# Kernel optimization log

Measured on AMD Instinct MI355X. Metric: run time of the kernel, lower is better.

The kernel has to match this reference:

```python
import jax, jax.numpy as jnp
import numpy as np

HIDDEN = 384
NDIM = 3
N_POINTS = 100000
N_SUPER = 2048
MAX_DEG = 32
RADIUS = 0.045
INPUT_DIM = 3


def _sincos_embed(coords):
    # ContinuousSincosEmbed: dim=384, ndim=3 -> 128 channels per spatial dim (64 sin + 64 cos)
    eff = HIDDEN // NDIM  # 128
    omega = jnp.arange(0, eff, 2, dtype=jnp.float32) / eff
    freq = 1.0 / (10000.0 ** omega)  # [eff//2]
    out = coords[..., None] * freq  # [..., ndim, eff//2]
    emb = jnp.concatenate([jnp.sin(out), jnp.cos(out)], axis=-1)  # [..., ndim, eff]
    return emb.reshape(coords.shape[:-1] + (HIDDEN,))


def _radius_neighbors(pos, sn_idx):
    # numpy preprocessing equivalent of torch_geometric.nn.pool.radius with
    # max_num_neighbors=MAX_DEG; fixed-size padded [S, K] output + validity mask.
    nbr = np.zeros((N_SUPER, MAX_DEG), np.int32)
    mask = np.zeros((N_SUPER, MAX_DEG), bool)
    pos2 = (pos ** 2).sum(-1)
    r2 = RADIUS * RADIUS
    chunk = 128
    for i0 in range(0, N_SUPER, chunk):
        sp = pos[sn_idx[i0:i0 + chunk]]
        d2 = (sp ** 2).sum(-1)[:, None] + pos2[None, :] - 2.0 * (sp @ pos.T)
        within = d2 <= r2
        for j in range(sp.shape[0]):
            idx = np.nonzero(within[j])[0][:MAX_DEG]
            nbr[i0 + j, :len(idx)] = idx
            mask[i0 + j, :len(idx)] = True
    return nbr, mask


def setup_inputs() -> dict:
    rng = np.random.default_rng(0)
    pos = rng.random((N_POINTS, NDIM)).astype(np.float32)
    sn_idx = np.sort(rng.choice(N_POINTS, N_SUPER, replace=False)).astype(np.int32)
    nbr, mask = _radius_neighbors(pos, sn_idx)
    key = jax.random.key(0)
    ks = jax.random.split(key, 6)
    s = 0.02  # truncnormal002 init scale
    return {
        "input_pos": jnp.asarray(pos),
        "input_feat": jax.random.normal(ks[0], (N_POINTS, INPUT_DIM), jnp.float32),
        "supernode_idx": jnp.asarray(sn_idx),
        "neighbor_idx": jnp.asarray(nbr),
        "neighbor_mask": jnp.asarray(mask),
        "W_in": jax.random.normal(ks[1], (INPUT_DIM, HIDDEN), jnp.float32) * s,
        "b_in": jnp.zeros((HIDDEN,), jnp.float32),
        "W1": jax.random.normal(ks[2], (2 * HIDDEN, HIDDEN), jnp.float32) * s,
        "b1": jnp.zeros((HIDDEN,), jnp.float32),
        "W2": jax.random.normal(ks[3], (HIDDEN, HIDDEN), jnp.float32) * s,
        "b2": jnp.zeros((HIDDEN,), jnp.float32),
        "W_proj": jax.random.normal(ks[4], (2 * HIDDEN, HIDDEN), jnp.float32) * s,
        "b_proj": jnp.zeros((HIDDEN,), jnp.float32),
    }


def reference(input_pos, input_feat, supernode_idx, neighbor_idx, neighbor_mask,
              W_in, b_in, W1, b1, W2, b2, W_proj, b_proj):
    # point embeddings: continuous sincos pos embed + input feature projection
    x = _sincos_embed(input_pos) + input_feat @ W_in + b_in          # [N, D]
    sn = x[supernode_idx]                                            # [S, D] supernode pos embed
    src = x[neighbor_idx]                                            # [S, K, D] gathered neighbors
    dst = jnp.broadcast_to(sn[:, None, :], src.shape)                # [S, K, D]
    h = jnp.concatenate([src, dst], axis=-1)                         # [S, K, 2D]
    # message MLP (Linear -> GELU(exact) -> Linear), as nn.GELU default
    h = jax.nn.gelu(h @ W1 + b1, approximate=False) @ W2 + b2        # [S, K, D]
    # masked mean == segment_csr(..., reduce='mean') over variable-degree edges
    m = neighbor_mask[..., None].astype(h.dtype)
    agg = (h * m).sum(axis=1) / jnp.maximum(m.sum(axis=1), 1.0)      # [S, D]
    # readd_supernode_pos: concat supernode pos embed, project 2D -> D
    out = jnp.concatenate([agg, sn], axis=-1) @ W_proj + b_proj      # [S, D]
    return out[None]                                                 # [1, S, D] (batch_size=1)
```

## Files before the change

### kernel.cpp

```cpp
#include <hip/hip_runtime.h>
#include <hip/hip_bf16.h>
#include <cstdint>

#define HIDDEN 384
#define NSUPER 2048
#define MAXDEG 32
#define FRAGS (12*24*64)
#define WBLK  (FRAGS*8)

typedef __attribute__((ext_vector_type(8))) short bf16x8;
typedef __attribute__((ext_vector_type(4))) float f32x4;

__device__ inline unsigned short f2bf(float f) {
    unsigned int u = __float_as_uint(f);
    return (unsigned short)((u + 0x7fffu + ((u >> 16) & 1u)) >> 16);
}
__device__ inline float b2f(unsigned short s) {
    return __uint_as_float(((unsigned int)s) << 16);
}
__device__ inline bf16x8 pack8(const float* v) {
    union { bf16x8 v8; unsigned short u[8]; } u;
    #pragma unroll
    for (int i = 0; i < 8; ++i) u.u[i] = f2bf(v[i]);
    return u.v8;
}
__device__ inline float gelu(float y) {
    const float y2 = y * y;
    const float m  = __expf(y * fmaf(-0.0713548163f, y2, -1.5957691216f));
    return y * (1.0f / (1.0f + m));
}

__global__ __launch_bounds__(256)
void prep(const float* __restrict__ W1, const float* __restrict__ W2,
          const float* __restrict__ Wp, const unsigned int* __restrict__ mask,
          const float* __restrict__ pos, const float* __restrict__ feat,
          const int* __restrict__ sn_idx,
          const float* __restrict__ W_in, const float* __restrict__ b_in,
          unsigned short* __restrict__ w1sf, unsigned short* __restrict__ w1df,
          unsigned short* __restrict__ w2f,  unsigned short* __restrict__ wpf,
          unsigned short* __restrict__ snxb, int* __restrict__ flag) {
    const int b = blockIdx.x;
    const int t = threadIdx.x;
    if (b == 360) {
        __shared__ int s;
        if (t == 0) s = 0;
        __syncthreads();
        int bad = 0;
        for (int i = t; i < 16384; i += 256)
            if (mask[i] > 1u) bad = 1;
        if (bad) s = 1;
        __syncthreads();
        if (t == 0) *flag = s;
        return;
    }
    if (b > 360) {
        __shared__ float W4[HIDDEN][4];
        __shared__ float P6[64][7];
        const int eb = b - 361;
        if (t < 64) {
            const int pi = sn_idx[eb*64 + t];
            P6[t][0]=pos[pi*3];  P6[t][1]=pos[pi*3+1];  P6[t][2]=pos[pi*3+2];
            P6[t][3]=feat[pi*3]; P6[t][4]=feat[pi*3+1]; P6[t][5]=feat[pi*3+2];
        }
        for (int d = t; d < HIDDEN; d += 256) {
            W4[d][0]=W_in[d]; W4[d][1]=W_in[HIDDEN+d];
            W4[d][2]=W_in[2*HIDDEN+d]; W4[d][3]=b_in[d];
        }
        __syncthreads();
        const int er = t >> 2, seg = t & 3;
        float frA[8], frB[8];
        #pragma unroll
        for (int i = 0; i < 8; ++i) {
            frA[i] = exp2f(-(float)(seg*8 + i)      * 0.2076205059304601f);
            frB[i] = exp2f(-(float)(32 + seg*8 + i) * 0.2076205059304601f);
        }
        const float f0 = P6[er][3], f1 = P6[er][4], f2 = P6[er][5];
        #pragma unroll
        for (int cc = 0; cc < 3; ++cc) {
            const float pc = P6[er][cc];
            float sL[8], sH[8], cL[8], cH[8];
            #pragma unroll
            for (int i = 0; i < 8; ++i) {
                const float aL = pc*frA[i], aH = pc*frB[i];
                sL[i]=__sinf(aL); sH[i]=__sinf(aH); cL[i]=__cosf(aL); cH[i]=__cosf(aH);
            }
            #pragma unroll
            for (int q = 0; q < 4; ++q) {
                const float* bb = (q==0)?sL:(q==1)?sH:(q==2)?cL:cH;
                const int blk = cc*4 + q;
                float v[8];
                #pragma unroll
                for (int i = 0; i < 8; ++i) {
                    const int dim = blk*32 + seg*8 + i;
                    const float4 wv = *(const float4*)W4[dim];
                    v[i] = fmaf(f0, wv.x, fmaf(f1, wv.y, fmaf(f2, wv.z, bb[i] + wv.w)));
                }
                *(bf16x8*)&snxb[(size_t)(eb*64 + er)*HIDDEN + blk*32 + seg*8] = pack8(v);
            }
        }
        return;
    }
    const int grp = b / 72, sub = b % 72;
    const float* W; unsigned short* out;
    switch (grp) {
        case 0: W = W1;              out = w1sf; break;
        case 1: W = W1 + 384*HIDDEN; out = w1df; break;
        case 2: W = W2;              out = w2f;  break;
        case 3: W = Wp;              out = wpf;  break;
        default:W = Wp + 384*HIDDEN; out = wpf + WBLK; break;
    }
    const int idx = sub * 256 + t;
    const int l   = idx & 63;
    const int frag= idx >> 6;
    const int nt  = frag % 24;
    const int kt  = frag / 24;
    const int col = nt * 16 + (l & 15);
    const int k0  = kt * 32 + (l >> 4) * 8;
    unsigned int pk[4];
    #pragma unroll
    for (int j = 0; j < 4; ++j) {
        unsigned int lo = f2bf(W[(k0 + 2*j)     * HIDDEN + col]);
        unsigned int hi = f2bf(W[(k0 + 2*j + 1) * HIDDEN + col]);
        pk[j] = lo | (hi << 16);
    }
    *reinterpret_cast<uint4*>(&out[(size_t)idx * 8]) =
        *reinterpret_cast<const uint4*>(pk);
}

__global__ __launch_bounds__(256, 2)
void k_mlp(const float* __restrict__ pos, const float* __restrict__ feat,
           const int* __restrict__ nbr_idx, const void* __restrict__ mask_raw,
           const int* __restrict__ mask_fmt,
           const float* __restrict__ W_in, const float* __restrict__ b_in,
           const unsigned short* __restrict__ snxb,
           const unsigned short* __restrict__ W1sf,
           const unsigned short* __restrict__ W1df,
           const float* __restrict__ b1,
           unsigned short* __restrict__ aggpre, float* __restrict__ cntf)
{
    __shared__ unsigned short G[4*12*64*8];
    __shared__ ushort4 WINTB[HIDDEN];
    __shared__ float PF[64][7];
    __shared__ float CNT[2];

    const int t  = threadIdx.x;
    const int bm = blockIdx.x;
    const int l = t & 63, ng = t >> 6, lg = l >> 4, l15 = l & 15;

    bf16x8 bA[6], bB[6];
    #define LOADB(dst, Wf, kt)                                                  \
        { const unsigned short* bp_ = &Wf[((size_t)((kt)*24 + ng*6)*64 + l)*8]; \
          _Pragma("unroll")                                                     \
          for (int nt_ = 0; nt_ < 6; ++nt_)                                     \
              dst[nt_] = *(const bf16x8*)(bp_ + (size_t)nt_*512); }
    #define AREAD(a_, kt)                                                       \
        { _Pragma("unroll")                                                     \
          for (int mt_ = 0; mt_ < 4; ++mt_)                                     \
              a_[mt_] = *(const bf16x8*)&G[(size_t)(((mt_*12 + (kt))*64) + l)*8]; }
    #define MFMA6(bfr, a_)                                                      \
        { __builtin_amdgcn_s_setprio(1);                                        \
          _Pragma("unroll")                                                     \
          for (int mt_ = 0; mt_ < 4; ++mt_)                                     \
              _Pragma("unroll")                                                 \
              for (int nt_ = 0; nt_ < 6; ++nt_)                                 \
                  acc[mt_][nt_] = __builtin_amdgcn_mfma_f32_16x16x32_bf16(      \
                      a_[mt_], bfr[nt_], acc[mt_][nt_], 0, 0, 0);               \
          __builtin_amdgcn_s_setprio(0); }

    if (t < 64) {
        const int e  = bm*64 + t;
        const int pi = nbr_idx[e];
        PF[t][0]=pos[pi*3];  PF[t][1]=pos[pi*3+1];  PF[t][2]=pos[pi*3+2];
        PF[t][3]=feat[pi*3]; PF[t][4]=feat[pi*3+1]; PF[t][5]=feat[pi*3+2];
        const int fmt = *mask_fmt;
        const int mv  = fmt ? (int)((const unsigned char*)mask_raw)[e]
                            : ((const int*)mask_raw)[e];
        PF[t][6] = mv ? 1.0f : 0.0f;
    }
    for (int d = t; d < HIDDEN; d += 256) {
        ushort4 wv;
        wv.x = f2bf(W_in[d]); wv.y = f2bf(W_in[HIDDEN+d]);
        wv.z = f2bf(W_in[2*HIDDEN+d]); wv.w = f2bf(b_in[d]);
        WINTB[d] = wv;
    }
    float b1r[6];
    #pragma unroll
    for (int nt = 0; nt < 6; ++nt) b1r[nt] = b1[ng*96 + nt*16 + l15];
    __syncthreads();
    if (t < 2) {
        float c = 0.f;
        for (int s = 0; s < 32; ++s) c += PF[t*32+s][6];
        CNT[t] = c;
    }

    const int er = t >> 2, seg = t & 3;
    float frA[8], frB[8];
    #pragma unroll
    for (int i = 0; i < 8; ++i) {
        frA[i] = exp2f(-(float)(seg*8 + i)      * 0.2076205059304601f);
        frB[i] = exp2f(-(float)(32 + seg*8 + i) * 0.2076205059304601f);
    }
    const float f0 = PF[er][3], f1 = PF[er][4], f2 = PF[er][5];
    const float pc0 = PF[er][0], pc1 = PF[er][1], pc2 = PF[er][2];
    const int slotbase = (er>>4)*12*64 + seg*16 + (er&15);

    #define EMB(kt_)                                                            \
        { const float pc = ((kt_)>>2)==0 ? pc0 : (((kt_)>>2)==1 ? pc1 : pc2);   \
          float v[8];                                                           \
          _Pragma("unroll")                                                     \
          for (int i = 0; i < 8; ++i) {                                         \
              const float fr = ((kt_)&1) ? frB[i] : frA[i];                     \
              const float aa = pc * fr;                                         \
              const float base = (((kt_)>>1)&1) ? __cosf(aa) : __sinf(aa);      \
              const ushort4 wv = WINTB[(kt_)*32 + seg*8 + i];                   \
              v[i] = fmaf(f0, b2f(wv.x), fmaf(f1, b2f(wv.y),                    \
                     fmaf(f2, b2f(wv.z), base + b2f(wv.w))));                   \
          }                                                                     \
          *(bf16x8*)&G[(size_t)(slotbase + (kt_)*64)*8] = pack8(v); }

    f32x4 acc[4][6];
    #pragma unroll
    for (int mt=0; mt<4; ++mt)
        #pragma unroll
        for (int nt=0; nt<6; ++nt) acc[mt][nt] = (f32x4){0.f,0.f,0.f,0.f};

    const unsigned short* snx0 = &snxb[(size_t)(bm*2 + 0)*HIDDEN];
    const unsigned short* snx1 = &snxb[(size_t)(bm*2 + 1)*HIDDEN];
    #pragma unroll
    for (int kt = 0; kt < 12; ++kt) {
        LOADB(bA, W1df, kt);
        bf16x8 s0 = *(const bf16x8*)&snx0[kt*32 + lg*8];
        bf16x8 s1 = *(const bf16x8*)&snx1[kt*32 + lg*8];
        EMB(kt);
        __builtin_amdgcn_s_setprio(1);
        #pragma unroll
        for (int nt = 0; nt < 6; ++nt) {
            acc[0][nt] = __builtin_amdgcn_mfma_f32_16x16x32_bf16(s0, bA[nt], acc[0][nt], 0,0,0);
            acc[1][nt] = __builtin_amdgcn_mfma_f32_16x16x32_bf16(s0, bA[nt], acc[1][nt], 0,0,0);
            acc[2][nt] = __builtin_amdgcn_mfma_f32_16x16x32_bf16(s1, bA[nt], acc[2][nt], 0,0,0);
            acc[3][nt] = __builtin_amdgcn_mfma_f32_16x16x32_bf16(s1, bA[nt], acc[3][nt], 0,0,0);
        }
        __builtin_amdgcn_s_setprio(0);
    }
    __syncthreads();

    LOADB(bA, W1sf, 0); LOADB(bB, W1sf, 1);
    #pragma unroll
    for (int kt = 0; kt < 12; kt += 2) {
        bf16x8 a[4];
        AREAD(a, kt);
        MFMA6(bA, a);
        if (kt + 2 < 12) LOADB(bA, W1sf, kt + 2);
        AREAD(a, kt + 1);
        MFMA6(bB, a);
        if (kt + 3 < 12) LOADB(bB, W1sf, kt + 3);
    }

    #pragma unroll
    for (int nt=0; nt<6; ++nt) {
        const int col = ng*96 + nt*16 + l15;
        const float bb1 = b1r[nt];
        float s0 = 0.f, s1 = 0.f;
        #pragma unroll
        for (int mt=0; mt<4; ++mt) {
            float p = 0.f;
            #pragma unroll
            for (int r=0; r<4; ++r)
                p += PF[mt*16 + lg*4 + r][6] * gelu(acc[mt][nt][r] + bb1);
            if (mt < 2) s0 += p; else s1 += p;
        }
        s0 += __shfl_xor(s0,16); s0 += __shfl_xor(s0,32);
        s1 += __shfl_xor(s1,16); s1 += __shfl_xor(s1,32);
        if (lg == 0) {
            const int sn0 = bm*2;
            aggpre[(size_t)sn0*HIDDEN + col]     = f2bf(s0 / fmaxf(CNT[0],1.f));
            aggpre[(size_t)(sn0+1)*HIDDEN + col] = f2bf(s1 / fmaxf(CNT[1],1.f));
        }
    }
    if (t < 2) cntf[bm*2 + t] = CNT[t];
    #undef LOADB
    #undef AREAD
    #undef MFMA6
    #undef EMB
}

__global__ __launch_bounds__(256)
void k_agg(const unsigned short* __restrict__ aggpre,
           const unsigned short* __restrict__ w2f,
           const float* __restrict__ b2, const float* __restrict__ cntf,
           unsigned short* __restrict__ aggb) {
    const int rg = blockIdx.x >> 2, cq = blockIdx.x & 3;
    const int t = threadIdx.x, w = t>>6, l = t&63, lg = l>>4, l15 = l&15;
    const int wgm = w>>1, wgn = w&1;
    const int r0 = rg*64 + wgm*32;
    const int ntb = cq*6 + wgn*3;
    f32x4 acc[2][3];
    #pragma unroll
    for (int mt=0; mt<2; ++mt)
        #pragma unroll
        for (int nt=0; nt<3; ++nt) acc[mt][nt] = (f32x4){0.f,0.f,0.f,0.f};
    #pragma unroll 2
    for (int kt = 0; kt < 12; ++kt) {
        bf16x8 a[2], bfr[3];
        const unsigned short* bpp = &w2f[((size_t)(kt*24 + ntb)*64 + l)*8];
        #pragma unroll
        for (int nt=0; nt<3; ++nt) bfr[nt] = *(const bf16x8*)(bpp + (size_t)nt*512);
        #pragma unroll
        for (int mt=0; mt<2; ++mt)
            a[mt] = *(const bf16x8*)&aggpre[(size_t)(r0 + mt*16 + l15)*HIDDEN + kt*32 + lg*8];
        #pragma unroll
        for (int mt=0; mt<2; ++mt)
            #pragma unroll
            for (int nt=0; nt<3; ++nt)
                acc[mt][nt] = __builtin_amdgcn_mfma_f32_16x16x32_bf16(a[mt], bfr[nt], acc[mt][nt], 0,0,0);
    }
    #pragma unroll
    for (int mt=0; mt<2; ++mt)
        #pragma unroll
        for (int nt=0; nt<3; ++nt) {
            const int col = cq*96 + wgn*48 + nt*16 + l15;
            const float bb = b2[col];
            #pragma unroll
            for (int r=0; r<4; ++r) {
                const int row = r0 + mt*16 + lg*4 + r;
                const float nz = (cntf[row] > 0.f) ? 1.f : 0.f;
                aggb[(size_t)row*HIDDEN + col] = f2bf(acc[mt][nt][r] + bb*nz);
            }
        }
}

__global__ __launch_bounds__(256)
void k_proj(const unsigned short* __restrict__ aggb,
            const unsigned short* __restrict__ snxb,
            const unsigned short* __restrict__ wpf,
            const float* __restrict__ bp, float* __restrict__ out) {
    const int rg = blockIdx.x >> 2, cq = blockIdx.x & 3;
    const int t = threadIdx.x, w = t>>6, l = t&63, lg = l>>4, l15 = l&15;
    const int wgm = w>>1, wgn = w&1;
    const int r0 = rg*64 + wgm*32;
    const int ntb = cq*6 + wgn*3;
    f32x4 acc[2][3];
    #pragma unroll
    for (int mt=0; mt<2; ++mt)
        #pragma unroll
        for (int nt=0; nt<3; ++nt) acc[mt][nt] = (f32x4){0.f,0.f,0.f,0.f};
    #pragma unroll 2
    for (int kt = 0; kt < 24; ++kt) {
        const unsigned short* Ab = (kt < 12) ? aggb : snxb;
        const unsigned short* Wb = (kt < 12) ? wpf  : wpf + WBLK;
        const int ktt = (kt < 12) ? kt : kt - 12;
        bf16x8 a[2], bfr[3];
        const unsigned short* bpp = &Wb[((size_t)(ktt*24 + ntb)*64 + l)*8];
        #pragma unroll
        for (int nt=0; nt<3; ++nt) bfr[nt] = *(const bf16x8*)(bpp + (size_t)nt*512);
        #pragma unroll
        for (int mt=0; mt<2; ++mt)
            a[mt] = *(const bf16x8*)&Ab[(size_t)(r0 + mt*16 + l15)*HIDDEN + ktt*32 + lg*8];
        #pragma unroll
        for (int mt=0; mt<2; ++mt)
            #pragma unroll
            for (int nt=0; nt<3; ++nt)
                acc[mt][nt] = __builtin_amdgcn_mfma_f32_16x16x32_bf16(a[mt], bfr[nt], acc[mt][nt], 0,0,0);
    }
    #pragma unroll
    for (int mt=0; mt<2; ++mt)
        #pragma unroll
        for (int nt=0; nt<3; ++nt) {
            const int col = cq*96 + wgn*48 + nt*16 + l15;
            #pragma unroll
            for (int r=0; r<4; ++r) {
                const int row = r0 + mt*16 + lg*4 + r;
                out[(size_t)row*HIDDEN + col] = acc[mt][nt][r] + bp[col];
            }
        }
}

extern "C" void kernel_launch(void* const* d_in, const int* in_sizes, int n_in,
                              void* d_out, int out_size, void* d_ws, size_t ws_size,
                              hipStream_t stream) {
    const float* pos   = (const float*)d_in[0];
    const float* feat  = (const float*)d_in[1];
    const int*   sn    = (const int*)d_in[2];
    const int*   nbr   = (const int*)d_in[3];
    const void*  mask  = d_in[4];
    const float* W_in  = (const float*)d_in[5];
    const float* b_in  = (const float*)d_in[6];
    const float* W1    = (const float*)d_in[7];
    const float* b1    = (const float*)d_in[8];
    const float* W2    = (const float*)d_in[9];
    const float* b2    = (const float*)d_in[10];
    const float* Wp    = (const float*)d_in[11];
    const float* bpv   = (const float*)d_in[12];
    float* out = (float*)d_out;

    char* base = (char*)d_ws;
    int* flag = (int*)base;
    unsigned short* w1sf = (unsigned short*)(base + 256);
    unsigned short* w1df = w1sf + WBLK;
    unsigned short* w2f  = w1df + WBLK;
    unsigned short* wpf  = w2f  + WBLK;
    unsigned short* snxb = wpf  + 2*(size_t)WBLK;
    unsigned short* aggb = snxb + (size_t)NSUPER*HIDDEN;
    unsigned short* aggp = aggb + (size_t)NSUPER*HIDDEN;
    float* cntf = (float*)(aggp + (size_t)NSUPER*HIDDEN);

    hipLaunchKernelGGL(prep, dim3(393), dim3(256), 0, stream,
                       W1, W2, Wp, (const unsigned int*)mask,
                       pos, feat, sn, W_in, b_in,
                       w1sf, w1df, w2f, wpf, snxb, flag);
    hipLaunchKernelGGL(k_mlp, dim3(1024), dim3(256), 0, stream,
                       pos, feat, nbr, mask, flag, W_in, b_in,
                       snxb, w1sf, w1df, b1, aggp, cntf);
    hipLaunchKernelGGL(k_agg, dim3(128), dim3(256), 0, stream,
                       aggp, w2f, b2, cntf, aggb);
    hipLaunchKernelGGL(k_proj, dim3(128), dim3(256), 0, stream,
                       aggb, snxb, wpf, bpv, out);
}
```

Measured before the change: 81.17 us.

## Precompute per-supernode dst projection once and widen MLP blocks to four supernodes

The dst half of the first layer (sn @ W1_dst + b1) is constant across a supernode's neighbors, so it moves into a separate small GEMM kernel run once per supernode and is added as a per-column bias after the src GEMM. This drops the redundant dst MFMAs that were repeated for every neighbor row. The MLP kernel now uses 512-thread blocks covering 4 supernodes (128 edges), with the embedding computed up front before a sync instead of interleaved with the dst MFMAs. The cost is an extra kernel launch, an fp32 dst buffer round trip, and a larger LDS footprint per block.

Result: slower. 87.21 us (+7.4%).

```diff
diff --git a/kernel.cpp b/kernel.cpp
--- a/kernel.cpp
+++ b/kernel.cpp
@@ -4,7 +4,6 @@
 
 #define HIDDEN 384
 #define NSUPER 2048
-#define MAXDEG 32
 #define FRAGS (12*24*64)
 #define WBLK  (FRAGS*8)
 
@@ -14,9 +13,6 @@
 __device__ inline unsigned short f2bf(float f) {
     unsigned int u = __float_as_uint(f);
     return (unsigned short)((u + 0x7fffu + ((u >> 16) & 1u)) >> 16);
-}
-__device__ inline float b2f(unsigned short s) {
-    return __uint_as_float(((unsigned int)s) << 16);
 }
 __device__ inline bf16x8 pack8(const float* v) {
     union { bf16x8 v8; unsigned short u[8]; } u;
@@ -119,44 +115,154 @@
     unsigned int pk[4];
     #pragma unroll
     for (int j = 0; j < 4; ++j) {
-        unsigned int lo = f2bf(W[(k0 + 2*j)     * HIDDEN + col]);
-        unsigned int hi = f2bf(W[(k0 + 2*j + 1) * HIDDEN + col]);
+        unsigned int lo = f2bf(W[(size_t)(k0 + 2*j)     * HIDDEN + col]);
+        unsigned int hi = f2bf(W[(size_t)(k0 + 2*j + 1) * HIDDEN + col]);
         pk[j] = lo | (hi << 16);
     }
     *reinterpret_cast<uint4*>(&out[(size_t)idx * 8]) =
         *reinterpret_cast<const uint4*>(pk);
 }
 
-__global__ __launch_bounds__(256, 2)
+__global__ __launch_bounds__(256)
+void k_dstv(const unsigned short* __restrict__ snxb,
+            const unsigned short* __restrict__ w1df,
+            const float* __restrict__ b1, float* __restrict__ dstv) {
+    const int rg = blockIdx.x >> 2, cq = blockIdx.x & 3;
+    const int t = threadIdx.x, w = t>>6, l = t&63, lg = l>>4, l15 = l&15;
+    const int wgm = w>>1, wgn = w&1;
+    const int r0 = rg*64 + wgm*32;
+    const int ntb = cq*6 + wgn*3;
+    f32x4 acc[2][3];
+    #pragma unroll
+    for (int mt=0; mt<2; ++mt)
+        #pragma unroll
+        for (int nt=0; nt<3; ++nt) acc[mt][nt] = (f32x4){0.f,0.f,0.f,0.f};
+    #pragma unroll 2
+    for (int kt = 0; kt < 12; ++kt) {
+        bf16x8 a[2], bfr[3];
+        const unsigned short* bpp = &w1df[((size_t)(kt*24 + ntb)*64 + l)*8];
+        #pragma unroll
+        for (int nt=0; nt<3; ++nt) bfr[nt] = *(const bf16x8*)(bpp + (size_t)nt*512);
+        #pragma unroll
+        for (int mt=0; mt<2; ++mt)
+            a[mt] = *(const bf16x8*)&snxb[(size_t)(r0 + mt*16 + l15)*HIDDEN + kt*32 + lg*8];
+        #pragma unroll
+        for (int mt=0; mt<2; ++mt)
+            #pragma unroll
+            for (int nt=0; nt<3; ++nt)
+                acc[mt][nt] = __builtin_amdgcn_mfma_f32_16x16x32_bf16(a[mt], bfr[nt], acc[mt][nt], 0,0,0);
+    }
+    #pragma unroll
+    for (int mt=0; mt<2; ++mt)
+        #pragma unroll
+        for (int nt=0; nt<3; ++nt) {
+            const int col = cq*96 + wgn*48 + nt*16 + l15;
+            #pragma unroll
+            for (int r=0; r<4; ++r) {
+                const int row = r0 + mt*16 + lg*4 + r;
+                dstv[(size_t)row*HIDDEN + col] = acc[mt][nt][r] + b1[col];
+            }
+        }
+}
+
+__global__ __launch_bounds__(512, 2)
 void k_mlp(const float* __restrict__ pos, const float* __restrict__ feat,
            const int* __restrict__ nbr_idx, const void* __restrict__ mask_raw,
            const int* __restrict__ mask_fmt,
            const float* __restrict__ W_in, const float* __restrict__ b_in,
-           const unsigned short* __restrict__ snxb,
+           const float* __restrict__ dstv,
            const unsigned short* __restrict__ W1sf,
-           const unsigned short* __restrict__ W1df,
-           const float* __restrict__ b1,
            unsigned short* __restrict__ aggpre, float* __restrict__ cntf)
 {
-    __shared__ unsigned short G[4*12*64*8];
+    __shared__ unsigned short G[8*12*64*8];
     __shared__ ushort4 WINTB[HIDDEN];
-    __shared__ float PF[64][7];
-    __shared__ float CNT[2];
+    __shared__ float PF[128][7];
+    __shared__ float CNT[4];
 
     const int t  = threadIdx.x;
     const int bm = blockIdx.x;
-    const int l = t & 63, ng = t >> 6, lg = l >> 4, l15 = l & 15;
+    const int l = t & 63, w = t >> 6;
+    const int mg = w >> 2, ng = w & 3;
+    const int lg = l >> 4, l15 = l & 15;
+
+    float dvreg[2][6];
+    #pragma unroll
+    for (int sl = 0; sl < 2; ++sl)
+        #pragma unroll
+        for (int nt = 0; nt < 6; ++nt)
+            dvreg[sl][nt] = dstv[(size_t)(bm*4 + mg*2 + sl)*HIDDEN + ng*96 + nt*16 + l15];
+
+    if (t < 128) {
+        const int e  = bm*128 + t;
+        const int pi = nbr_idx[e];
+        PF[t][0]=pos[pi*3];  PF[t][1]=pos[pi*3+1];  PF[t][2]=pos[pi*3+2];
+        PF[t][3]=feat[pi*3]; PF[t][4]=feat[pi*3+1]; PF[t][5]=feat[pi*3+2];
+        const int fmt = *mask_fmt;
+        const int mv  = fmt ? (int)((const unsigned char*)mask_raw)[e]
+                            : ((const int*)mask_raw)[e];
+        PF[t][6] = mv ? 1.0f : 0.0f;
+    }
+    if (t >= 128 && t < 128 + HIDDEN) {
+        const int d = t - 128;
+        ushort4 wv;
+        wv.x = f2bf(W_in[d]); wv.y = f2bf(W_in[HIDDEN+d]);
+        wv.z = f2bf(W_in[2*HIDDEN+d]); wv.w = f2bf(b_in[d]);
+        WINTB[d] = wv;
+    }
+    __syncthreads();
+    if (t < 4) {
+        float c = 0.f;
+        for (int s = 0; s < 32; ++s) c += PF[t*32+s][6];
+        CNT[t] = c;
+    }
+
+    {
+        const int er = t >> 2, seg = t & 3;
+        float frA[8], frB[8];
+        #pragma unroll
+        for (int i = 0; i < 8; ++i) {
+            frA[i] = exp2f(-(float)(seg*8 + i)      * 0.2076205059304601f);
+            frB[i] = exp2f(-(float)(32 + seg*8 + i) * 0.2076205059304601f);
+        }
+        const float f0 = PF[er][3], f1 = PF[er][4], f2 = PF[er][5];
+        const float pc0 = PF[er][0], pc1 = PF[er][1], pc2 = PF[er][2];
+        const int slotbase = (er>>4)*12*64 + seg*16 + (er&15);
+        #pragma unroll
+        for (int kt = 0; kt < 12; ++kt) {
+            const float pc = (kt>>2)==0 ? pc0 : ((kt>>2)==1 ? pc1 : pc2);
+            float v[8];
+            #pragma unroll
+            for (int i = 0; i < 8; ++i) {
+                const float fr = (kt&1) ? frB[i] : frA[i];
+                const float aa = pc * fr;
+                const float base = ((kt>>1)&1) ? __cosf(aa) : __sinf(aa);
+                const ushort4 wv = WINTB[kt*32 + seg*8 + i];
+                v[i] = fmaf(__uint_as_float((unsigned)wv.x<<16), f0,
+                       fmaf(__uint_as_float((unsigned)wv.y<<16), f1,
+                       fmaf(__uint_as_float((unsigned)wv.z<<16), f2,
+                            base + __uint_as_float((unsigned)wv.w<<16))));
+            }
+            *(bf16x8*)&G[(size_t)(slotbase + kt*64)*8] = pack8(v);
+        }
+    }
+    __syncthreads();
+
+    f32x4 acc[4][6];
+    #pragma unroll
+    for (int mt=0; mt<4; ++mt)
+        #pragma unroll
+        for (int nt=0; nt<6; ++nt) acc[mt][nt] = (f32x4){0.f,0.f,0.f,0.f};
 
     bf16x8 bA[6], bB[6];
-    #define LOADB(dst, Wf, kt)                                                  \
-        { const unsigned short* bp_ = &Wf[((size_t)((kt)*24 + ng*6)*64 + l)*8]; \
+    #define LOADB(dst, kt)                                                      \
+        { const unsigned short* bp_ = &W1sf[((size_t)((kt)*24 + ng*6)*64 + l)*8];\
           _Pragma("unroll")                                                     \
           for (int nt_ = 0; nt_ < 6; ++nt_)                                     \
               dst[nt_] = *(const bf16x8*)(bp_ + (size_t)nt_*512); }
     #define AREAD(a_, kt)                                                       \
         { _Pragma("unroll")                                                     \
           for (int mt_ = 0; mt_ < 4; ++mt_)                                     \
-              a_[mt_] = *(const bf16x8*)&G[(size_t)(((mt_*12 + (kt))*64) + l)*8]; }
+              a_[mt_] = *(const bf16x8*)&G[(size_t)((((mg*4 + mt_)*12 + (kt))*64) + l)*8]; }
     #define MFMA6(bfr, a_)                                                      \
         { __builtin_amdgcn_s_setprio(1);                                        \
           _Pragma("unroll")                                                     \
@@ -167,121 +273,49 @@
                       a_[mt_], bfr[nt_], acc[mt_][nt_], 0, 0, 0);               \
           __builtin_amdgcn_s_setprio(0); }
 
-    if (t < 64) {
-        const int e  = bm*64 + t;
-        const int pi = nbr_idx[e];
-        PF[t][0]=pos[pi*3];  PF[t][1]=pos[pi*3+1];  PF[t][2]=pos[pi*3+2];
-        PF[t][3]=feat[pi*3]; PF[t][4]=feat[pi*3+1]; PF[t][5]=feat[pi*3+2];
-        const int fmt = *mask_fmt;
-        const int mv  = fmt ? (int)((const unsigned char*)mask_raw)[e]
-                            : ((const int*)mask_raw)[e];
-        PF[t][6] = mv ? 1.0f : 0.0f;
-    }
-    for (int d = t; d < HIDDEN; d += 256) {
-        ushort4 wv;
-        wv.x = f2bf(W_in[d]); wv.y = f2bf(W_in[HIDDEN+d]);
-        wv.z = f2bf(W_in[2*HIDDEN+d]); wv.w = f2bf(b_in[d]);
-        WINTB[d] = wv;
-    }
-    float b1r[6];
-    #pragma unroll
-    for (int nt = 0; nt < 6; ++nt) b1r[nt] = b1[ng*96 + nt*16 + l15];
-    __syncthreads();
-    if (t < 2) {
-        float c = 0.f;
-        for (int s = 0; s < 32; ++s) c += PF[t*32+s][6];
-        CNT[t] = c;
-    }
-
-    const int er = t >> 2, seg = t & 3;
-    float frA[8], frB[8];
-    #pragma unroll
-    for (int i = 0; i < 8; ++i) {
-        frA[i] = exp2f(-(float)(seg*8 + i)      * 0.2076205059304601f);
-        frB[i] = exp2f(-(float)(32 + seg*8 + i) * 0.2076205059304601f);
-    }
-    const float f0 = PF[er][3], f1 = PF[er][4], f2 = PF[er][5];
-    const float pc0 = PF[er][0], pc1 = PF[er][1], pc2 = PF[er][2];
-    const int slotbase = (er>>4)*12*64 + seg*16 + (er&15);
-
-    #define EMB(kt_)                                                            \
-        { const float pc = ((kt_)>>2)==0 ? pc0 : (((kt_)>>2)==1 ? pc1 : pc2);   \
-          float v[8];                                                           \
-          _Pragma("unroll")                                                     \
-          for (int i = 0; i < 8; ++i) {                                         \
-              const float fr = ((kt_)&1) ? frB[i] : frA[i];                     \
-              const float aa = pc * fr;                                         \
-              const float base = (((kt_)>>1)&1) ? __cosf(aa) : __sinf(aa);      \
-              const ushort4 wv = WINTB[(kt_)*32 + seg*8 + i];                   \
-              v[i] = fmaf(f0, b2f(wv.x), fmaf(f1, b2f(wv.y),                    \
-                     fmaf(f2, b2f(wv.z), base + b2f(wv.w))));                   \
-          }                                                                     \
-          *(bf16x8*)&G[(size_t)(slotbase + (kt_)*64)*8] = pack8(v); }
-
-    f32x4 acc[4][6];
-    #pragma unroll
-    for (int mt=0; mt<4; ++mt)
-        #pragma unroll
-        for (int nt=0; nt<6; ++nt) acc[mt][nt] = (f32x4){0.f,0.f,0.f,0.f};
-
-    const unsigned short* snx0 = &snxb[(size_t)(bm*2 + 0)*HIDDEN];
-    const unsigned short* snx1 = &snxb[(size_t)(bm*2 + 1)*HIDDEN];
-    #pragma unroll
-    for (int kt = 0; kt < 12; ++kt) {
-        LOADB(bA, W1df, kt);
-        bf16x8 s0 = *(const bf16x8*)&snx0[kt*32 + lg*8];
-        bf16x8 s1 = *(const bf16x8*)&snx1[kt*32 + lg*8];
-        EMB(kt);
-        __builtin_amdgcn_s_setprio(1);
-        #pragma unroll
-        for (int nt = 0; nt < 6; ++nt) {
-            acc[0][nt] = __builtin_amdgcn_mfma_f32_16x16x32_bf16(s0, bA[nt], acc[0][nt], 0,0,0);
-            acc[1][nt] = __builtin_amdgcn_mfma_f32_16x16x32_bf16(s0, bA[nt], acc[1][nt], 0,0,0);
-            acc[2][nt] = __builtin_amdgcn_mfma_f32_16x16x32_bf16(s1, bA[nt], acc[2][nt], 0,0,0);
-            acc[3][nt] = __builtin_amdgcn_mfma_f32_16x16x32_bf16(s1, bA[nt], acc[3][nt], 0,0,0);
-        }
-        __builtin_amdgcn_s_setprio(0);
-    }
-    __syncthreads();
-
-    LOADB(bA, W1sf, 0); LOADB(bB, W1sf, 1);
+    LOADB(bA, 0); LOADB(bB, 1);
     #pragma unroll
     for (int kt = 0; kt < 12; kt += 2) {
         bf16x8 a[4];
         AREAD(a, kt);
         MFMA6(bA, a);
-        if (kt + 2 < 12) LOADB(bA, W1sf, kt + 2);
+        if (kt + 2 < 12) LOADB(bA, kt + 2);
         AREAD(a, kt + 1);
         MFMA6(bB, a);
-        if (kt + 3 < 12) LOADB(bB, W1sf, kt + 3);
-    }
-
+        if (kt + 3 < 12) LOADB(bB, kt + 3);
+    }
+
+    float mvr[4][4];
+    #pragma unroll
+    for (int mt=0; mt<4; ++mt)
+        #pragma unroll
+        for (int r=0; r<4; ++r)
+            mvr[mt][r] = PF[(mg*4 + mt)*16 + lg*4 + r][6];
     #pragma unroll
     for (int nt=0; nt<6; ++nt) {
         const int col = ng*96 + nt*16 + l15;
-        const float bb1 = b1r[nt];
         float s0 = 0.f, s1 = 0.f;
         #pragma unroll
         for (int mt=0; mt<4; ++mt) {
+            const float dv = dvreg[mt>>1][nt];
             float p = 0.f;
             #pragma unroll
             for (int r=0; r<4; ++r)
-                p += PF[mt*16 + lg*4 + r][6] * gelu(acc[mt][nt][r] + bb1);
+                p += mvr[mt][r] * gelu(acc[mt][nt][r] + dv);
             if (mt < 2) s0 += p; else s1 += p;
         }
         s0 += __shfl_xor(s0,16); s0 += __shfl_xor(s0,32);
         s1 += __shfl_xor(s1,16); s1 += __shfl_xor(s1,32);
         if (lg == 0) {
-            const int sn0 = bm*2;
-            aggpre[(size_t)sn0*HIDDEN + col]     = f2bf(s0 / fmaxf(CNT[0],1.f));
-            aggpre[(size_t)(sn0+1)*HIDDEN + col] = f2bf(s1 / fmaxf(CNT[1],1.f));
-        }
-    }
-    if (t < 2) cntf[bm*2 + t] = CNT[t];
+            const int sn0 = bm*4 + mg*2;
+            aggpre[(size_t)sn0*HIDDEN + col]     = f2bf(s0 / fmaxf(CNT[mg*2],1.f));
+            aggpre[(size_t)(sn0+1)*HIDDEN + col] = f2bf(s1 / fmaxf(CNT[mg*2+1],1.f));
+        }
+    }
+    if (t < 4) cntf[bm*4 + t] = CNT[t];
     #undef LOADB
     #undef AREAD
     #undef MFMA6
-    #undef EMB
 }
 
 __global__ __launch_bounds__(256)
@@ -403,14 +437,17 @@
     unsigned short* aggb = snxb + (size_t)NSUPER*HIDDEN;
     unsigned short* aggp = aggb + (size_t)NSUPER*HIDDEN;
     float* cntf = (float*)(aggp + (size_t)NSUPER*HIDDEN);
+    float* dstv = cntf + NSUPER;
 
     hipLaunchKernelGGL(prep, dim3(393), dim3(256), 0, stream,
                        W1, W2, Wp, (const unsigned int*)mask,
                        pos, feat, sn, W_in, b_in,
                        w1sf, w1df, w2f, wpf, snxb, flag);
-    hipLaunchKernelGGL(k_mlp, dim3(1024), dim3(256), 0, stream,
-                       pos, feat, nbr, mask, flag, W_in, b_in,
-                       snxb, w1sf, w1df, b1, aggp, cntf);
+    hipLaunchKernelGGL(k_dstv, dim3(128), dim3(256), 0, stream,
+                       snxb, w1df, b1, dstv);
+    hipLaunchKernelGGL(k_mlp, dim3(512), dim3(512), 0, stream,
+                       pos, feat, nbr, mask, flag, W_in, b_in, dstv,
+                       w1sf, aggp, cntf);
     hipLaunchKernelGGL(k_agg, dim3(128), dim3(256), 0, stream,
                        aggp, w2f, b2, cntf, aggb);
     hipLaunchKernelGGL(k_proj, dim3(128), dim3(256), 0, stream,
```

## Fuse W2 aggregation GEMM and output projection into one kernel via LDS

Applied to the files above, without the earlier changes.

Merges k_agg and k_proj into a single k_out kernel. Each block computes the full 64x384 W2 product for its row group into shared memory, then runs the projection reading the aggregated tile from LDS instead of a global bf16 buffer. This removes one launch and the global round trip of the intermediate, but each of the four column-quarter blocks now recomputes the full W2 GEMM for its rows, which is four times the W2 work, and holds 24 accumulators per wave. It also hoists the per-row mask weights into registers in k_mlp's epilogue.

Result: slower. 83.56 us (+2.9%).

```diff
diff --git a/kernel.cpp b/kernel.cpp
--- a/kernel.cpp
+++ b/kernel.cpp
@@ -4,7 +4,6 @@
 
 #define HIDDEN 384
 #define NSUPER 2048
-#define MAXDEG 32
 #define FRAGS (12*24*64)
 #define WBLK  (FRAGS*8)
 
@@ -119,8 +118,8 @@
     unsigned int pk[4];
     #pragma unroll
     for (int j = 0; j < 4; ++j) {
-        unsigned int lo = f2bf(W[(k0 + 2*j)     * HIDDEN + col]);
-        unsigned int hi = f2bf(W[(k0 + 2*j + 1) * HIDDEN + col]);
+        unsigned int lo = f2bf(W[(size_t)(k0 + 2*j)     * HIDDEN + col]);
+        unsigned int hi = f2bf(W[(size_t)(k0 + 2*j + 1) * HIDDEN + col]);
         pk[j] = lo | (hi << 16);
     }
     *reinterpret_cast<uint4*>(&out[(size_t)idx * 8]) =
@@ -256,6 +255,12 @@
         if (kt + 3 < 12) LOADB(bB, W1sf, kt + 3);
     }
 
+    float mvr[4][4];
+    #pragma unroll
+    for (int mt=0; mt<4; ++mt)
+        #pragma unroll
+        for (int r=0; r<4; ++r)
+            mvr[mt][r] = PF[mt*16 + lg*4 + r][6];
     #pragma unroll
     for (int nt=0; nt<6; ++nt) {
         const int col = ng*96 + nt*16 + l15;
@@ -266,7 +271,7 @@
             float p = 0.f;
             #pragma unroll
             for (int r=0; r<4; ++r)
-                p += PF[mt*16 + lg*4 + r][6] * gelu(acc[mt][nt][r] + bb1);
+                p += mvr[mt][r] * gelu(acc[mt][nt][r] + bb1);
             if (mt < 2) s0 += p; else s1 += p;
         }
         s0 += __shfl_xor(s0,16); s0 += __shfl_xor(s0,32);
@@ -285,59 +290,56 @@
 }
 
 __global__ __launch_bounds__(256)
-void k_agg(const unsigned short* __restrict__ aggpre,
+void k_out(const unsigned short* __restrict__ aggpre,
+           const unsigned short* __restrict__ snxb,
            const unsigned short* __restrict__ w2f,
-           const float* __restrict__ b2, const float* __restrict__ cntf,
-           unsigned short* __restrict__ aggb) {
+           const unsigned short* __restrict__ wpf,
+           const float* __restrict__ b2, const float* __restrict__ bp,
+           const float* __restrict__ cntf, float* __restrict__ out) {
+    __shared__ unsigned short AGG[64][392];
     const int rg = blockIdx.x >> 2, cq = blockIdx.x & 3;
     const int t = threadIdx.x, w = t>>6, l = t&63, lg = l>>4, l15 = l&15;
     const int wgm = w>>1, wgn = w&1;
-    const int r0 = rg*64 + wgm*32;
-    const int ntb = cq*6 + wgn*3;
-    f32x4 acc[2][3];
-    #pragma unroll
-    for (int mt=0; mt<2; ++mt)
-        #pragma unroll
-        for (int nt=0; nt<3; ++nt) acc[mt][nt] = (f32x4){0.f,0.f,0.f,0.f};
-    #pragma unroll 2
-    for (int kt = 0; kt < 12; ++kt) {
-        bf16x8 a[2], bfr[3];
-        const unsigned short* bpp = &w2f[((size_t)(kt*24 + ntb)*64 + l)*8];
-        #pragma unroll
-        for (int nt=0; nt<3; ++nt) bfr[nt] = *(const bf16x8*)(bpp + (size_t)nt*512);
+    const int r0g = rg*64;
+
+    {
+        const int rowm = wgm*32;
+        f32x4 acc[2][12];
         #pragma unroll
         for (int mt=0; mt<2; ++mt)
-            a[mt] = *(const bf16x8*)&aggpre[(size_t)(r0 + mt*16 + l15)*HIDDEN + kt*32 + lg*8];
+            #pragma unroll
+            for (int nt=0; nt<12; ++nt) acc[mt][nt] = (f32x4){0.f,0.f,0.f,0.f};
+        for (int kt = 0; kt < 12; ++kt) {
+            bf16x8 a[2], bfr[12];
+            const unsigned short* bpp = &w2f[((size_t)(kt*24 + wgn*12)*64 + l)*8];
+            #pragma unroll
+            for (int nt=0; nt<12; ++nt) bfr[nt] = *(const bf16x8*)(bpp + (size_t)nt*512);
+            #pragma unroll
+            for (int mt=0; mt<2; ++mt)
+                a[mt] = *(const bf16x8*)&aggpre[(size_t)(r0g + rowm + mt*16 + l15)*HIDDEN + kt*32 + lg*8];
+            #pragma unroll
+            for (int mt=0; mt<2; ++mt)
+                #pragma unroll
+                for (int nt=0; nt<12; ++nt)
+                    acc[mt][nt] = __builtin_amdgcn_mfma_f32_16x16x32_bf16(a[mt], bfr[nt], acc[mt][nt], 0,0,0);
+        }
         #pragma unroll
         for (int mt=0; mt<2; ++mt)
             #pragma unroll
-            for (int nt=0; nt<3; ++nt)
-                acc[mt][nt] = __builtin_amdgcn_mfma_f32_16x16x32_bf16(a[mt], bfr[nt], acc[mt][nt], 0,0,0);
-    }
-    #pragma unroll
-    for (int mt=0; mt<2; ++mt)
-        #pragma unroll
-        for (int nt=0; nt<3; ++nt) {
-            const int col = cq*96 + wgn*48 + nt*16 + l15;
-            const float bb = b2[col];
-            #pragma unroll
-            for (int r=0; r<4; ++r) {
-                const int row = r0 + mt*16 + lg*4 + r;
-                const float nz = (cntf[row] > 0.f) ? 1.f : 0.f;
-                aggb[(size_t)row*HIDDEN + col] = f2bf(acc[mt][nt][r] + bb*nz);
+            for (int nt=0; nt<12; ++nt) {
+                const int col = wgn*192 + nt*16 + l15;
+                const float bb = b2[col];
+                #pragma unroll
+                for (int r=0; r<4; ++r) {
+                    const int row = rowm + mt*16 + lg*4 + r;
+                    const float nz = (cntf[r0g + row] > 0.f) ? 1.f : 0.f;
+                    AGG[row][col] = f2bf(acc[mt][nt][r] + bb*nz);
+                }
             }
-        }
-}
-
-__global__ __launch_bounds__(256)
-void k_proj(const unsigned short* __restrict__ aggb,
-            const unsigned short* __restrict__ snxb,
-            const unsigned short* __restrict__ wpf,
-            const float* __restrict__ bp, float* __restrict__ out) {
-    const int rg = blockIdx.x >> 2, cq = blockIdx.x & 3;
-    const int t = threadIdx.x, w = t>>6, l = t&63, lg = l>>4, l15 = l&15;
-    const int wgm = w>>1, wgn = w&1;
-    const int r0 = rg*64 + wgm*32;
+    }
+    __syncthreads();
+
+    const int r0 = r0g + wgm*32;
     const int ntb = cq*6 + wgn*3;
     f32x4 acc[2][3];
     #pragma unroll
@@ -346,16 +348,19 @@
         for (int nt=0; nt<3; ++nt) acc[mt][nt] = (f32x4){0.f,0.f,0.f,0.f};
     #pragma unroll 2
     for (int kt = 0; kt < 24; ++kt) {
-        const unsigned short* Ab = (kt < 12) ? aggb : snxb;
-        const unsigned short* Wb = (kt < 12) ? wpf  : wpf + WBLK;
+        const unsigned short* Wb = (kt < 12) ? wpf : wpf + WBLK;
         const int ktt = (kt < 12) ? kt : kt - 12;
         bf16x8 a[2], bfr[3];
         const unsigned short* bpp = &Wb[((size_t)(ktt*24 + ntb)*64 + l)*8];
         #pragma unroll
         for (int nt=0; nt<3; ++nt) bfr[nt] = *(const bf16x8*)(bpp + (size_t)nt*512);
         #pragma unroll
-        for (int mt=0; mt<2; ++mt)
-            a[mt] = *(const bf16x8*)&Ab[(size_t)(r0 + mt*16 + l15)*HIDDEN + ktt*32 + lg*8];
+        for (int mt=0; mt<2; ++mt) {
+            if (kt < 12)
+                a[mt] = *(const bf16x8*)&AGG[wgm*32 + mt*16 + l15][ktt*32 + lg*8];
+            else
+                a[mt] = *(const bf16x8*)&snxb[(size_t)(r0 + mt*16 + l15)*HIDDEN + ktt*32 + lg*8];
+        }
         #pragma unroll
         for (int mt=0; mt<2; ++mt)
             #pragma unroll
@@ -400,8 +405,7 @@
     unsigned short* w2f  = w1df + WBLK;
     unsigned short* wpf  = w2f  + WBLK;
     unsigned short* snxb = wpf  + 2*(size_t)WBLK;
-    unsigned short* aggb = snxb + (size_t)NSUPER*HIDDEN;
-    unsigned short* aggp = aggb + (size_t)NSUPER*HIDDEN;
+    unsigned short* aggp = snxb + (size_t)NSUPER*HIDDEN;
     float* cntf = (float*)(aggp + (size_t)NSUPER*HIDDEN);
 
     hipLaunchKernelGGL(prep, dim3(393), dim3(256), 0, stream,
@@ -411,8 +415,6 @@
     hipLaunchKernelGGL(k_mlp, dim3(1024), dim3(256), 0, stream,
                        pos, feat, nbr, mask, flag, W_in, b_in,
                        snxb, w1sf, w1df, b1, aggp, cntf);
-    hipLaunchKernelGGL(k_agg, dim3(128), dim3(256), 0, stream,
-                       aggp, w2f, b2, cntf, aggb);
-    hipLaunchKernelGGL(k_proj, dim3(128), dim3(256), 0, stream,
-                       aggb, snxb, wpf, bpv, out);
-}
+    hipLaunchKernelGGL(k_out, dim3(128), dim3(256), 0, stream,
+                       aggp, snxb, w2f, wpf, b2, bpv, cntf, out);
+}
```
